# Performance work log

Hardware: AMD Instinct MI355X
Metric: run time of the kernel (lower is better)

Reference implementation:

```python
import jax, jax.numpy as jnp
import numpy as np

B, T, C, H = 8, 2048, 1024, 128

def setup_inputs() -> dict:
    key = jax.random.key(0)
    kx, kq, kk, kv = jax.random.split(key, 4)
    x = jax.random.normal(kx, (B, T, C), dtype=jnp.float32)
    Wq = jax.random.normal(kq, (C, H), dtype=jnp.float32) * 0.02
    Wk = jax.random.normal(kk, (C, H), dtype=jnp.float32) * 0.02
    Wv = jax.random.normal(kv, (C, H), dtype=jnp.float32) * 0.02
    return {"x": x, "Wq": Wq, "Wk": Wk, "Wv": Wv}

def reference(x, Wq, Wk, Wv):
    # q,k,v: [B,T,H] via bias-free dense projections
    q = jnp.einsum('btc,ch->bth', x, Wq)
    k = jnp.einsum('btc,ch->bth', x, Wk)
    v = jnp.einsum('btc,ch->bth', x, Wv)
    scale = k.shape[-1] ** (-0.5)
    # scores: [B,T,T]
    wei = jnp.einsum('bth,bsh->bts', q, k) * scale
    Tlen = x.shape[1]
    causal = jnp.tril(jnp.ones((Tlen, Tlen), dtype=bool))  # True = keep
    wei = jnp.where(causal[None, :, :], wei, -jnp.inf)
    wei = jax.nn.softmax(wei, axis=-1)
    return jnp.einsum('bts,bsh->bth', wei, v)
```

## Files before the change

### kernel.cpp

```cpp
#include <hip/hip_runtime.h>

#define B_ 8
#define T_ 2048
#define C_ 1024
#define H_ 128
#define BT_ (B_*T_)

typedef unsigned short u16;
typedef unsigned int u32;
typedef __attribute__((ext_vector_type(4))) float f32x4;
typedef __attribute__((ext_vector_type(8))) __bf16 bf16x8;

__device__ __forceinline__ u16 f2bf(float f) {
  u32 u = __float_as_uint(f);
  u += 0x7fffu + ((u >> 16) & 1u);
  return (u16)(u >> 16);
}

__device__ __forceinline__ bf16x8 load_frag(const u16* base, int stride, int row0, int k0, int lane) {
  const u16* p = base + (size_t)(row0 + (lane & 15)) * stride + k0 + ((lane >> 4) << 3);
  return *reinterpret_cast<const bf16x8*>(p);
}

__global__ void wt_kernel(const float* __restrict__ Wq, const float* __restrict__ Wk,
                          const float* __restrict__ Wv, u16* __restrict__ wt) {
  int mat = blockIdx.y;
  const float* W = (mat == 0) ? Wq : (mat == 1) ? Wk : Wv;
  int i = blockIdx.x * 256 + threadIdx.x;
  int h = i >> 10;
  int c = i & 1023;
  wt[mat * (C_ * H_) + i] = f2bf(W[c * H_ + h]);
}

__global__ __launch_bounds__(256) void qkv_gemm(const float* __restrict__ x, const u16* __restrict__ wt,
                                                u16* __restrict__ q, u16* __restrict__ k2,
                                                u16* __restrict__ vt) {
  __shared__ __align__(16) u16 As[2][64 * 40];
  __shared__ __align__(16) u16 Bs[2][128 * 40];
  int t = threadIdx.x;
  int lane = t & 63, w = t >> 6;
  int wm = w >> 1, wn = w & 1;
  int quad = lane >> 4, col = lane & 15;
  int m0 = blockIdx.x * 64;
  int mat = blockIdx.y;
  const u16* wmp = wt + mat * (C_ * H_);

  int ar = t >> 2, ac = (t & 3) * 8;
  int br = t >> 2, bc = (t & 3) * 8;

  {
    const float* ap = x + (size_t)(m0 + ar) * C_ + ac;
    float4 a4 = *reinterpret_cast<const float4*>(ap);
    float4 a5 = *reinterpret_cast<const float4*>(ap + 4);
    union { u16 h[8]; uint4 v; } ah;
    ah.h[0] = f2bf(a4.x); ah.h[1] = f2bf(a4.y); ah.h[2] = f2bf(a4.z); ah.h[3] = f2bf(a4.w);
    ah.h[4] = f2bf(a5.x); ah.h[5] = f2bf(a5.y); ah.h[6] = f2bf(a5.z); ah.h[7] = f2bf(a5.w);
    *reinterpret_cast<uint4*>(&As[0][ar * 40 + ac]) = ah.v;
#pragma unroll
    for (int p = 0; p < 2; p++)
      *reinterpret_cast<uint4*>(&Bs[0][(br + 64 * p) * 40 + bc]) =
          *reinterpret_cast<const uint4*>(wmp + (size_t)(br + 64 * p) * C_ + bc);
  }

  f32x4 acc[2][4] = {};
  for (int kk = 0; kk < 32; kk++) {
    int cur = kk & 1;
    __syncthreads();
    bool more = (kk + 1 < 32);
    float4 a4, a5; uint4 b4[2];
    if (more) {
      int kn = (kk + 1) * 32;
      const float* ap = x + (size_t)(m0 + ar) * C_ + kn + ac;
      a4 = *reinterpret_cast<const float4*>(ap);
      a5 = *reinterpret_cast<const float4*>(ap + 4);
#pragma unroll
      for (int p = 0; p < 2; p++)
        b4[p] = *reinterpret_cast<const uint4*>(wmp + (size_t)(br + 64 * p) * C_ + kn + bc);
    }
    const u16* A = &As[cur][0];
    const u16* Bb = &Bs[cur][0];
    bf16x8 af[2], bfr[4];
#pragma unroll
    for (int mt = 0; mt < 2; mt++)
      af[mt] = *reinterpret_cast<const bf16x8*>(&A[(wm * 32 + mt * 16 + col) * 40 + quad * 8]);
#pragma unroll
    for (int nt = 0; nt < 4; nt++)
      bfr[nt] = *reinterpret_cast<const bf16x8*>(&Bb[(wn * 64 + nt * 16 + col) * 40 + quad * 8]);
#pragma unroll
    for (int mt = 0; mt < 2; mt++)
#pragma unroll
      for (int nt = 0; nt < 4; nt++)
        acc[mt][nt] = __builtin_amdgcn_mfma_f32_16x16x32_bf16(af[mt], bfr[nt], acc[mt][nt], 0, 0, 0);
    if (more) {
      int nxt = cur ^ 1;
      union { u16 h[8]; uint4 v; } ah;
      ah.h[0] = f2bf(a4.x); ah.h[1] = f2bf(a4.y); ah.h[2] = f2bf(a4.z); ah.h[3] = f2bf(a4.w);
      ah.h[4] = f2bf(a5.x); ah.h[5] = f2bf(a5.y); ah.h[6] = f2bf(a5.z); ah.h[7] = f2bf(a5.w);
      *reinterpret_cast<uint4*>(&As[nxt][ar * 40 + ac]) = ah.v;
#pragma unroll
      for (int p = 0; p < 2; p++)
        *reinterpret_cast<uint4*>(&Bs[nxt][(br + 64 * p) * 40 + bc]) = b4[p];
    }
  }

#pragma unroll
  for (int mt = 0; mt < 2; mt++) {
#pragma unroll
    for (int nt = 0; nt < 4; nt++) {
#pragma unroll
      for (int r = 0; r < 4; r++) {
        int row = m0 + wm * 32 + mt * 16 + quad * 4 + r;
        int n = wn * 64 + nt * 16 + col;
        u16 val = f2bf(acc[mt][nt][r]);
        if (mat == 0) {
          q[(size_t)row * H_ + n] = val;
        } else if (mat == 1) {
          k2[(size_t)row * H_ + n] = val;
        } else {
          int bb = row >> 11;
          int tt = row & 2047;
          vt[((size_t)bb * H_ + n) * T_ + tt] = val;
        }
      }
    }
  }
}

__global__ __launch_bounds__(256) void attn_part(const u16* __restrict__ q, const u16* __restrict__ k,
                                                 const u16* __restrict__ vt,
                                                 float* __restrict__ Op, float* __restrict__ lsum) {
  __shared__ __align__(16) u16 Ks[2][32 * 136];
  __shared__ __align__(16) u16 Vs[2][128 * 40];
  __shared__ __align__(16) u16 P[4][2][16 * 40];
  int t = threadIdx.x;
  int lane = t & 63, w = t >> 6;
  int quad = lane >> 4, col = lane & 15;
  int bx = blockIdx.x;
  int qt = 31 - (bx >> 4);
  int s = (bx >> 3) & 1;
  int b = bx & 7;
  const float scale = 0.08838834764831845f;

  int nk = 2 * (qt + 1);
  int n0 = qt + 1;
  int it0 = s ? n0 : 0;
  int it1 = s ? nk : n0;

  int krow0 = t >> 4, ke = (t & 15) * 8;
  int krow1 = krow0 + 16;
  int vrow0 = t >> 2, ve = (t & 3) * 8;
  int vrow1 = vrow0 + 64;

  int qrow0 = b * T_ + qt * 64 + w * 16;
  bf16x8 qf[4];
#pragma unroll
  for (int ks = 0; ks < 4; ks++) qf[ks] = load_frag(q, H_, qrow0, ks * 32, lane);

  f32x4 o[8] = {};
  float l[4] = {0.f, 0.f, 0.f, 0.f};
  int myqrow = qt * 64 + w * 16 + quad * 4;

  {
    const u16* kb = k + (size_t)(b * T_ + it0 * 32) * H_;
    *reinterpret_cast<uint4*>(&Ks[0][krow0 * 136 + ke]) = *reinterpret_cast<const uint4*>(kb + (size_t)krow0 * 128 + ke);
    *reinterpret_cast<uint4*>(&Ks[0][krow1 * 136 + ke]) = *reinterpret_cast<const uint4*>(kb + (size_t)krow1 * 128 + ke);
    const u16* vb = vt + (size_t)b * H_ * T_ + it0 * 32;
    *reinterpret_cast<uint4*>(&Vs[0][vrow0 * 40 + ve]) = *reinterpret_cast<const uint4*>(vb + (size_t)vrow0 * T_ + ve);
    *reinterpret_cast<uint4*>(&Vs[0][vrow1 * 40 + ve]) = *reinterpret_cast<const uint4*>(vb + (size_t)vrow1 * T_ + ve);
  }

  for (int kt = it0; kt < it1; kt++) {
    int cur = (kt - it0) & 1;
    __syncthreads();
    bool more = (kt + 1 < it1);
    uint4 kc0, kc1, vc0, vc1;
    if (more) {
      const u16* kb = k + (size_t)(b * T_ + (kt + 1) * 32) * H_;
      kc0 = *reinterpret_cast<const uint4*>(kb + (size_t)krow0 * 128 + ke);
      kc1 = *reinterpret_cast<const uint4*>(kb + (size_t)krow1 * 128 + ke);
      const u16* vb = vt + (size_t)b * H_ * T_ + (kt + 1) * 32;
      vc0 = *reinterpret_cast<const uint4*>(vb + (size_t)vrow0 * T_ + ve);
      vc1 = *reinterpret_cast<const uint4*>(vb + (size_t)vrow1 * T_ + ve);
    }

    f32x4 s0 = {}, s1 = {};
#pragma unroll
    for (int ks = 0; ks < 4; ks++) {
      bf16x8 kb0 = *reinterpret_cast<const bf16x8*>(&Ks[cur][col * 136 + ks * 32 + quad * 8]);
      bf16x8 kb1 = *reinterpret_cast<const bf16x8*>(&Ks[cur][(col + 16) * 136 + ks * 32 + quad * 8]);
      s0 = __builtin_amdgcn_mfma_f32_16x16x32_bf16(qf[ks], kb0, s0, 0, 0, 0);
      s1 = __builtin_amdgcn_mfma_f32_16x16x32_bf16(qf[ks], kb1, s1, 0, 0, 0);
    }

    float pv[8];
    int kcol0 = kt * 32 + col;
#pragma unroll
    for (int r = 0; r < 4; r++) {
      int qr = myqrow + r;
      float a0 = fminf(s0[r] * scale, 30.f);
      float a1 = fminf(s1[r] * scale, 30.f);
      a0 = (kcol0      > qr) ? -1e30f : a0;
      a1 = (kcol0 + 16 > qr) ? -1e30f : a1;
      float p0 = __expf(a0);
      float p1 = __expf(a1);
      pv[r] = p0; pv[4 + r] = p1;
      l[r] += p0 + p1;
    }

    u16* Pb = &P[w][cur][0];
#pragma unroll
    for (int r = 0; r < 4; r++) {
      Pb[(quad * 4 + r) * 40 + col] = f2bf(pv[r]);
      Pb[(quad * 4 + r) * 40 + col + 16] = f2bf(pv[4 + r]);
    }
    asm volatile("" ::: "memory");
    __builtin_amdgcn_s_waitcnt(0xc07f);
    asm volatile("" ::: "memory");
    bf16x8 pf = *reinterpret_cast<const bf16x8*>(&Pb[col * 40 + (quad << 3)]);

#pragma unroll
    for (int ht = 0; ht < 8; ht++) {
      bf16x8 vf = *reinterpret_cast<const bf16x8*>(&Vs[cur][(ht * 16 + col) * 40 + quad * 8]);
      o[ht] = __builtin_amdgcn_mfma_f32_16x16x32_bf16(pf, vf, o[ht], 0, 0, 0);
    }

    if (more) {
      int nxt = cur ^ 1;
      *reinterpret_cast<uint4*>(&Ks[nxt][krow0 * 136 + ke]) = kc0;
      *reinterpret_cast<uint4*>(&Ks[nxt][krow1 * 136 + ke]) = kc1;
      *reinterpret_cast<uint4*>(&Vs[nxt][vrow0 * 40 + ve]) = vc0;
      *reinterpret_cast<uint4*>(&Vs[nxt][vrow1 * 40 + ve]) = vc1;
    }
  }

#pragma unroll
  for (int r = 0; r < 4; r++) {
    float v = l[r];
    v += __shfl_xor(v, 1);
    v += __shfl_xor(v, 2);
    v += __shfl_xor(v, 4);
    v += __shfl_xor(v, 8);
    l[r] = v;
  }

  int tile = (s * 8 + b) * 32 + qt;
  float* Orow = Op + (size_t)tile * (64 * 128);
  float* lrow = lsum + (size_t)tile * 64;
  int rowin0 = w * 16 + quad * 4;
  if (col == 0) {
#pragma unroll
    for (int r = 0; r < 4; r++) lrow[rowin0 + r] = l[r];
  }
#pragma unroll
  for (int ht = 0; ht < 8; ht++) {
#pragma unroll
    for (int r = 0; r < 4; r++)
      Orow[(size_t)(rowin0 + r) * 128 + ht * 16 + col] = o[ht][r];
  }
}

__global__ __launch_bounds__(256) void attn_comb(const float* __restrict__ Op, const float* __restrict__ lsum,
                                                 float* __restrict__ out) {
  int bx = blockIdx.x;
  int b = bx >> 5, qt = bx & 31;
  int t = threadIdx.x;
  int h = t & 127, half = t >> 7;
  int tile0 = b * 32 + qt;
  int tile1 = tile0 + 256;
#pragma unroll 4
  for (int rr = 0; rr < 32; rr++) {
    int row = half * 32 + rr;
    float l0 = lsum[tile0 * 64 + row];
    float l1 = lsum[tile1 * 64 + row];
    float rl = 1.f / (l0 + l1);
    float v = (Op[(size_t)tile0 * 8192 + row * 128 + h] +
               Op[(size_t)tile1 * 8192 + row * 128 + h]) * rl;
    out[((size_t)(b * T_ + qt * 64 + row)) * H_ + h] = v;
  }
}

extern "C" void kernel_launch(void* const* d_in, const int* in_sizes, int n_in,
                              void* d_out, int out_size, void* d_ws, size_t ws_size,
                              hipStream_t stream) {
  (void)in_sizes; (void)n_in; (void)out_size; (void)ws_size;
  const float* x  = (const float*)d_in[0];
  const float* Wq = (const float*)d_in[1];
  const float* Wk = (const float*)d_in[2];
  const float* Wv = (const float*)d_in[3];
  u16* ws = (u16*)d_ws;
  u16* q  = ws;
  u16* k  = ws + (size_t)BT_ * H_;
  u16* vt = ws + 2 * (size_t)BT_ * H_;
  u16* wt = ws + 3 * (size_t)BT_ * H_;
  float* Op = (float*)(ws + 3 * (size_t)BT_ * H_ + 3 * C_ * H_);
  float* lsum = Op + (size_t)512 * 64 * 128;
  float* out = (float*)d_out;

  wt_kernel<<<dim3(512, 3), 256, 0, stream>>>(Wq, Wk, Wv, wt);
  qkv_gemm<<<dim3(BT_ / 64, 3), 256, 0, stream>>>(x, wt, q, k, vt);
  attn_part<<<dim3(512), 256, 0, stream>>>(q, k, vt, Op, lsum);
  attn_comb<<<dim3(256), 256, 0, stream>>>(Op, lsum, out);
}
```

Baseline: 172.1 us.

## Fuse Q/K/V projections into one GEMM block using direct global-to-LDS loads

```diff
diff --git a/kernel.cpp b/kernel.cpp
--- a/kernel.cpp
+++ b/kernel.cpp
@@ -17,9 +17,20 @@
   return (u16)(u >> 16);
 }
 
+#define GLL16(g, l) __builtin_amdgcn_global_load_lds( \
+    (const __attribute__((address_space(1))) void*)(g), \
+    (__attribute__((address_space(3))) void*)(l), 16, 0, 0)
+
 __device__ __forceinline__ bf16x8 load_frag(const u16* base, int stride, int row0, int k0, int lane) {
   const u16* p = base + (size_t)(row0 + (lane & 15)) * stride + k0 + ((lane >> 4) << 3);
   return *reinterpret_cast<const bf16x8*>(p);
+}
+
+__device__ __forceinline__ bf16x8 cvt8(f32x4 lo, f32x4 hi) {
+  union { u16 h[8]; bf16x8 v; } u;
+#pragma unroll
+  for (int i = 0; i < 4; i++) { u.h[i] = f2bf(lo[i]); u.h[4 + i] = f2bf(hi[i]); }
+  return u.v;
 }
 
 __global__ void wt_kernel(const float* __restrict__ Wq, const float* __restrict__ Wk,
@@ -32,95 +43,82 @@
   wt[mat * (C_ * H_) + i] = f2bf(W[c * H_ + h]);
 }
 
-__global__ __launch_bounds__(256) void qkv_gemm(const float* __restrict__ x, const u16* __restrict__ wt,
+__global__ __launch_bounds__(512) void qkv_gemm(const float* __restrict__ x, const u16* __restrict__ wt,
                                                 u16* __restrict__ q, u16* __restrict__ k2,
                                                 u16* __restrict__ vt) {
-  __shared__ __align__(16) u16 As[2][64 * 40];
-  __shared__ __align__(16) u16 Bs[2][128 * 40];
+  __shared__ __align__(16) float As[2][64 * 32];
+  __shared__ __align__(16) u16 Bs[2][3 * 128 * 32];
   int t = threadIdx.x;
   int lane = t & 63, w = t >> 6;
-  int wm = w >> 1, wn = w & 1;
+  int wm = w >> 2, wn = w & 3;
   int quad = lane >> 4, col = lane & 15;
   int m0 = blockIdx.x * 64;
-  int mat = blockIdx.y;
-  const u16* wmp = wt + mat * (C_ * H_);
-
-  int ar = t >> 2, ac = (t & 3) * 8;
-  int br = t >> 2, bc = (t & 3) * 8;
-
-  {
-    const float* ap = x + (size_t)(m0 + ar) * C_ + ac;
-    float4 a4 = *reinterpret_cast<const float4*>(ap);
-    float4 a5 = *reinterpret_cast<const float4*>(ap + 4);
-    union { u16 h[8]; uint4 v; } ah;
-    ah.h[0] = f2bf(a4.x); ah.h[1] = f2bf(a4.y); ah.h[2] = f2bf(a4.z); ah.h[3] = f2bf(a4.w);
-    ah.h[4] = f2bf(a5.x); ah.h[5] = f2bf(a5.y); ah.h[6] = f2bf(a5.z); ah.h[7] = f2bf(a5.w);
-    *reinterpret_cast<uint4*>(&As[0][ar * 40 + ac]) = ah.v;
-#pragma unroll
-    for (int p = 0; p < 2; p++)
-      *reinterpret_cast<uint4*>(&Bs[0][(br + 64 * p) * 40 + bc]) =
-          *reinterpret_cast<const uint4*>(wmp + (size_t)(br + 64 * p) * C_ + bc);
-  }
-
-  f32x4 acc[2][4] = {};
+
+  int arow = t >> 3;
+  int agr = (t & 7) ^ (arow & 7);
+  const float* axg = x + (size_t)(m0 + arow) * C_ + agr * 4;
+  const u16* bwg = wt + (size_t)(t >> 2) * C_ + (t & 3) * 8;
+
+  GLL16(axg, &As[0][w * 256]);
+#pragma unroll
+  for (int p = 0; p < 3; p++)
+    GLL16(bwg + (size_t)p * 128 * C_, &Bs[0][p * 4096 + w * 512]);
+
+  f32x4 acc[2][6] = {};
   for (int kk = 0; kk < 32; kk++) {
-    int cur = kk & 1;
+    int cur = kk & 1, nxt = cur ^ 1;
     __syncthreads();
-    bool more = (kk + 1 < 32);
-    float4 a4, a5; uint4 b4[2];
-    if (more) {
+    if (kk + 1 < 32) {
       int kn = (kk + 1) * 32;
-      const float* ap = x + (size_t)(m0 + ar) * C_ + kn + ac;
-      a4 = *reinterpret_cast<const float4*>(ap);
-      a5 = *reinterpret_cast<const float4*>(ap + 4);
-#pragma unroll
-      for (int p = 0; p < 2; p++)
-        b4[p] = *reinterpret_cast<const uint4*>(wmp + (size_t)(br + 64 * p) * C_ + kn + bc);
-    }
-    const u16* A = &As[cur][0];
+      GLL16(axg + kn, &As[nxt][w * 256]);
+#pragma unroll
+      for (int p = 0; p < 3; p++)
+        GLL16(bwg + (size_t)p * 128 * C_ + kn, &Bs[nxt][p * 4096 + w * 512]);
+    }
+    const float* Ab = &As[cur][0];
     const u16* Bb = &Bs[cur][0];
-    bf16x8 af[2], bfr[4];
+    bf16x8 af[2];
+#pragma unroll
+    for (int mt = 0; mt < 2; mt++) {
+      int r = wm * 32 + mt * 16 + col;
+      int s0 = (quad * 2) ^ (r & 7);
+      int s1 = (quad * 2 + 1) ^ (r & 7);
+      f32x4 lo = *reinterpret_cast<const f32x4*>(Ab + r * 32 + s0 * 4);
+      f32x4 hi = *reinterpret_cast<const f32x4*>(Ab + r * 32 + s1 * 4);
+      af[mt] = cvt8(lo, hi);
+    }
+    bf16x8 bfr[6];
+#pragma unroll
+    for (int nt = 0; nt < 6; nt++) {
+      int n = wn * 96 + nt * 16 + col;
+      bfr[nt] = *reinterpret_cast<const bf16x8*>(Bb + n * 32 + quad * 8);
+    }
 #pragma unroll
     for (int mt = 0; mt < 2; mt++)
-      af[mt] = *reinterpret_cast<const bf16x8*>(&A[(wm * 32 + mt * 16 + col) * 40 + quad * 8]);
-#pragma unroll
-    for (int nt = 0; nt < 4; nt++)
-      bfr[nt] = *reinterpret_cast<const bf16x8*>(&Bb[(wn * 64 + nt * 16 + col) * 40 + quad * 8]);
-#pragma unroll
-    for (int mt = 0; mt < 2; mt++)
-#pragma unroll
-      for (int nt = 0; nt < 4; nt++)
+#pragma unroll
+      for (int nt = 0; nt < 6; nt++)
         acc[mt][nt] = __builtin_amdgcn_mfma_f32_16x16x32_bf16(af[mt], bfr[nt], acc[mt][nt], 0, 0, 0);
-    if (more) {
-      int nxt = cur ^ 1;
-      union { u16 h[8]; uint4 v; } ah;
-      ah.h[0] = f2bf(a4.x); ah.h[1] = f2bf(a4.y); ah.h[2] = f2bf(a4.z); ah.h[3] = f2bf(a4.w);
-      ah.h[4] = f2bf(a5.x); ah.h[5] = f2bf(a5.y); ah.h[6] = f2bf(a5.z); ah.h[7] = f2bf(a5.w);
-      *reinterpret_cast<uint4*>(&As[nxt][ar * 40 + ac]) = ah.v;
-#pragma unroll
-      for (int p = 0; p < 2; p++)
-        *reinterpret_cast<uint4*>(&Bs[nxt][(br + 64 * p) * 40 + bc]) = b4[p];
-    }
   }
 
 #pragma unroll
   for (int mt = 0; mt < 2; mt++) {
-#pragma unroll
-    for (int nt = 0; nt < 4; nt++) {
-#pragma unroll
-      for (int r = 0; r < 4; r++) {
-        int row = m0 + wm * 32 + mt * 16 + quad * 4 + r;
-        int n = wn * 64 + nt * 16 + col;
-        u16 val = f2bf(acc[mt][nt][r]);
-        if (mat == 0) {
-          q[(size_t)row * H_ + n] = val;
-        } else if (mat == 1) {
-          k2[(size_t)row * H_ + n] = val;
-        } else {
-          int bb = row >> 11;
-          int tt = row & 2047;
-          vt[((size_t)bb * H_ + n) * T_ + tt] = val;
-        }
+    int row0 = m0 + wm * 32 + mt * 16 + quad * 4;
+#pragma unroll
+    for (int nt = 0; nt < 6; nt++) {
+      int n = wn * 96 + nt * 16 + col;
+      int mat = n >> 7, h = n & 127;
+      if (mat == 0) {
+#pragma unroll
+        for (int r = 0; r < 4; r++) q[(size_t)(row0 + r) * H_ + h] = f2bf(acc[mt][nt][r]);
+      } else if (mat == 1) {
+#pragma unroll
+        for (int r = 0; r < 4; r++) k2[(size_t)(row0 + r) * H_ + h] = f2bf(acc[mt][nt][r]);
+      } else {
+        int bb = row0 >> 11, tt = row0 & 2047;
+        ushort4 pk;
+        pk.x = f2bf(acc[mt][nt][0]); pk.y = f2bf(acc[mt][nt][1]);
+        pk.z = f2bf(acc[mt][nt][2]); pk.w = f2bf(acc[mt][nt][3]);
+        *reinterpret_cast<ushort4*>(&vt[((size_t)bb * H_ + h) * T_ + tt]) = pk;
       }
     }
   }
@@ -297,7 +295,7 @@
   float* out = (float*)d_out;
 
   wt_kernel<<<dim3(512, 3), 256, 0, stream>>>(Wq, Wk, Wv, wt);
-  qkv_gemm<<<dim3(BT_ / 64, 3), 256, 0, stream>>>(x, wt, q, k, vt);
+  qkv_gemm<<<dim3(256), 512, 0, stream>>>(x, wt, q, k, vt);
   attn_part<<<dim3(512), 256, 0, stream>>>(q, k, vt, Op, lsum);
   attn_comb<<<dim3(256), 256, 0, stream>>>(Op, lsum, out);
 }
```

Measured after the change: 180.9 us. 5.1% more time.
